# Kernel optimization log

Measured on AMD Instinct MI355X. Metric: run time of the kernel, lower is better.

Reference implementation:

```python
import jax, jax.numpy as jnp
import numpy as np

B, S, D, K = 16, 1024, 512, 4
DIL = (1, 2, 4, 8)
EPS_BN = 1e-5
EPS_LN = 1e-5


def _edge_conv1d(x, w, b, dilation):
    # x: [B, C, S], w: [O, C, k]; replicate ('edge') padding keeps length S
    p = (w.shape[-1] - 1) * dilation // 2
    xp = jnp.pad(x, ((0, 0), (0, 0), (p, p)), mode='edge')
    y = jax.lax.conv_general_dilated(xp, w, (1,), 'VALID', rhs_dilation=(dilation,),
                                     dimension_numbers=('NCH', 'OIH', 'NCH'))
    return y + b[None, :, None]


def setup_inputs() -> dict:
    key = jax.random.key(0)
    ks = jax.random.split(key, 16)
    g = lambda i, shape, s: jax.random.normal(ks[i], shape, jnp.float32) * s
    return {
        'x': g(0, (B, S, D), 1.0),
        'conv_w': g(1, (4, D, D, 3), 0.02),
        'conv_b': jnp.zeros((4, D), jnp.float32),
        'fusion_w': g(2, (D, 4 * D), 0.02),
        'fusion_b': jnp.zeros((D,), jnp.float32),
        'refine_w': g(3, (D, D, 3), 0.02),
        'refine_b': jnp.zeros((D,), jnp.float32),
        'hyp1_w': g(4, (D, D, 3), 0.02),
        'hyp1_b': jnp.zeros((D,), jnp.float32),
        'bn_gamma': jnp.ones((D,), jnp.float32),
        'bn_beta': jnp.zeros((D,), jnp.float32),
        'hyp2_w': g(5, (D // 2, D, 3), 0.02),
        'hyp2_b': jnp.zeros((D // 2,), jnp.float32),
        'proj_w': g(6, (2 * K, D // 2), 0.05),
        'proj_b': jnp.zeros((2 * K,), jnp.float32),
        'gate_w': g(7, (D, D), 0.02),
        'gate_b': jnp.zeros((D,), jnp.float32),
        'base_w': g(8, (D, D), 0.02),
        'base_b': jnp.zeros((D,), jnp.float32),
        'wav_w': g(9, (K, D, D), 0.02),
        'wav_b': jnp.zeros((K, D), jnp.float32),
        'ln_gamma': jnp.ones((D,), jnp.float32),
        'ln_beta': jnp.zeros((D,), jnp.float32),
    }


def _forward(x, conv_w, conv_b, fusion_w, fusion_b, refine_w, refine_b,
             hyp1_w, hyp1_b, bn_gamma, bn_beta, hyp2_w, hyp2_b,
             proj_w, proj_b, gate_w, gate_b, base_w, base_b,
             wav_w, wav_b, ln_gamma, ln_beta):
    residual = x
    x_in = jnp.transpose(x, (0, 2, 1))                      # [B, D, S]
    # ---- FFT trend/seasonal split ----
    fx = jnp.fft.rfft(x_in, axis=2)
    cutoff = S // 10
    mask = (jnp.arange(fx.shape[2]) < cutoff).astype(fx.dtype)
    x_seasonal = jnp.fft.irfft(fx * mask, n=S, axis=2)       # [B, D, S]
    x_smooth = x_seasonal
    x_spike = x_in - x_seasonal
    # ---- iterative dilated-conv smoothing (dropout = identity, eval mode) ----
    for _ in range(2):  # iterations
        outs = [jax.nn.gelu(_edge_conv1d(x_smooth, conv_w[i], conv_b[i], DIL[i]),
                            approximate=False)
                for i in range(4)]
        x_concat = jnp.concatenate(outs, axis=1)             # [B, 4D, S]
        x_smooth = jnp.einsum('oc,bcs->bos', fusion_w, x_concat) + fusion_b[None, :, None]
        x_spike = _edge_conv1d(x_in - x_smooth, refine_w, refine_b, 1)
    x_smooth_t = jnp.transpose(x_smooth, (0, 2, 1))          # [B, S, D]
    x_spike_t = jnp.transpose(x_spike, (0, 2, 1))            # [B, S, D]
    # ---- hypernet (BatchNorm in eval mode: running mean 0, var 1) ----
    h = _edge_conv1d(x_smooth, hyp1_w, hyp1_b, 1)
    h = h / jnp.sqrt(1.0 + EPS_BN) * bn_gamma[None, :, None] + bn_beta[None, :, None]
    h = jax.nn.silu(h)
    h = jax.nn.silu(_edge_conv1d(h, hyp2_w, hyp2_b, 1))      # [B, D/2, S]
    cnn_feat = jnp.mean(h, axis=2)                           # AdaptiveAvgPool1d(1)
    params = (cnn_feat @ proj_w.T + proj_b).reshape(B, 1, K, 2)
    dyn_a = jax.nn.softplus(params[..., 0]) + 0.01           # [B, 1, K]
    dyn_b = jax.nn.sigmoid(params[..., 1]) * S               # [B, 1, K]
    # ---- wavelet-KAN base path: Linear(silu(x_smooth)) ----
    base_out = jnp.einsum('bsd,ed->bse', jax.nn.silu(x_smooth_t), base_w) + base_b
    # ---- wavelet path: mexican-hat wavelets over sequence positions ----
    pos = jnp.arange(S, dtype=x.dtype)[None, :, None]        # [1, S, 1]
    u = (pos - dyn_b) / dyn_a                                # [B, S, K]
    c = 2.0 / (np.sqrt(3.0) * np.pi ** 0.25)
    psi = c * (1.0 - u * u) * jnp.exp(-0.5 * u * u)          # [B, S, K]
    z = jnp.einsum('bsd,kde->bkse', x_spike_t, wav_w)        # per-wavelet linear
    kan_out = jnp.einsum('bsk,bkse->bse', psi, z) + jnp.einsum('bsk,ke->bse', psi, wav_b)
    amp = jax.nn.sigmoid(base_out @ gate_w.T + gate_b) * 2.0
    x_out = base_out + kan_out * amp
    # ---- residual + LayerNorm ----
    y = x_out + residual
    mu = jnp.mean(y, axis=-1, keepdims=True)
    var = jnp.var(y, axis=-1, keepdims=True)
    return (y - mu) / jnp.sqrt(var + EPS_LN) * ln_gamma + ln_beta


def reference(x, conv_w, conv_b, fusion_w, fusion_b, refine_w, refine_b,
              hyp1_w, hyp1_b, bn_gamma, bn_beta, hyp2_w, hyp2_b,
              proj_w, proj_b, gate_w, gate_b, base_w, base_b,
              wav_w, wav_b, ln_gamma, ln_beta):
    return _forward(x, conv_w, conv_b, fusion_w, fusion_b, refine_w, refine_b,
                    hyp1_w, hyp1_b, bn_gamma, bn_beta, hyp2_w, hyp2_b,
                    proj_w, proj_b, gate_w, gate_b, base_w, base_b,
                    wav_w, wav_b, ln_gamma, ln_beta)
```

## Files before the change

kernel.cpp:

```cpp
#include <hip/hip_runtime.h>
#include <hip/hip_bf16.h>
#include <math.h>

#define NB 16
#define SS 1024
#define DD 512
#define HD 256

typedef unsigned short US;
typedef short bf16x8 __attribute__((ext_vector_type(8)));
typedef float f32x4 __attribute__((ext_vector_type(4)));
typedef __attribute__((address_space(1))) const void gv1;
typedef __attribute__((address_space(3))) void lv3;

static __device__ __forceinline__ float b2sf(US u){ return __uint_as_float(((unsigned)u)<<16); }
static __device__ __forceinline__ US f2b(float f){
  __hip_bfloat16 h = __float2bfloat16(f);
  union { __hip_bfloat16 h; US u; } c; c.h = h; return c.u;
}
static __device__ __forceinline__ float rd(const void* __restrict__ p, long i, int isf){
  return isf ? ((const float*)p)[i] : b2sf(((const US*)p)[i]);
}

__global__ void k_detect(const void* __restrict__ x, int* __restrict__ flag){
  const US* u = (const US*)x;
  int t = threadIdx.x;
  float m = 0.f;
  for (int i = t; i < 4096; i += 256){
    float v = fabsf(b2sf(u[i]));
    if (isnan(v) || isinf(v)) v = 1e30f;
    m = fmaxf(m, v);
  }
  for (int off = 32; off; off >>= 1) m = fmaxf(m, __shfl_down(m, off));
  __shared__ float sh[4];
  if ((t & 63) == 0) sh[t >> 6] = m;
  __syncthreads();
  if (t == 0){
    float mm = fmaxf(fmaxf(sh[0], sh[1]), fmaxf(sh[2], sh[3]));
    flag[0] = (mm > 1e6f) ? 1 : 0;
  }
}

struct WTab { const void* src[8]; long start[9]; int type[8]; int C[8]; };
__global__ void k_prep_w(WTab wt, US* __restrict__ dst, const int* __restrict__ fl){
  int isf = fl[0];
  long i = (long)blockIdx.x*256 + threadIdx.x;
  if (i >= wt.start[8]) return;
  int s = 0;
  while (i >= wt.start[s+1]) s++;
  long r = i - wt.start[s];
  long si;
  if (wt.type[s] == 0){
    int C = wt.C[s]; long oc3 = 3L*C;
    int o = (int)(r / oc3); int rr = (int)(r - (long)o*oc3); int t = rr / C; int c = rr - t*C;
    si = ((long)o*C + c)*3 + t;
  } else if (wt.type[s] == 1){
    int k = (int)(r >> 18); int e = (int)((r >> 9) & 511); int d = (int)(r & 511);
    si = ((long)(k*512 + d))*512 + e;
  } else si = r;
  dst[i] = f2b(rd(wt.src[s], si, isf));
}

struct FTab { const void* src[14]; int start[15]; };
__global__ void k_cvt_all(FTab ft, float* __restrict__ dst, const int* __restrict__ fl){
  int isf = fl[0];
  int i = blockIdx.x*256 + threadIdx.x;
  if (i >= ft.start[14]) return;
  int s = 0;
  while (i >= ft.start[s+1]) s++;
  dst[i] = rd(ft.src[s], i - ft.start[s], isf);
}

__global__ void k_build_g(float* __restrict__ g){
  int d = blockIdx.x*256 + threadIdx.x;
  if (d >= SS) return;
  float s = 1.f;
  for (int k = 1; k < 102; ++k){
    int r = (k*d) & (SS-1);
    s += 2.f * cosf(6.28318530718f * (float)r * (1.f/SS));
  }
  g[d] = s * (1.f/SS);
}
__global__ void k_build_cmat(const float* __restrict__ g, US* __restrict__ cm){
  int i = blockIdx.x*256 + threadIdx.x;
  if (i >= SS*SS) return;
  int t = i >> 10, s = i & (SS-1);
  cm[i] = f2b(g[(s - t) & (SS-1)]);
}
__global__ __launch_bounds__(256) void k_transpose_b(const void* __restrict__ x, US* __restrict__ xt, const int* __restrict__ fl){
  int isf = fl[0];
  __shared__ float tl[32][33];
  int b = blockIdx.z, s0 = blockIdx.x*32, d0 = blockIdx.y*32;
  int tx = threadIdx.x & 31, ty = threadIdx.x >> 5;
  for (int i = ty; i < 32; i += 8)
    tl[i][tx] = rd(x, ((long)(b*SS + s0+i))*DD + d0+tx, isf);
  __syncthreads();
  for (int i = ty; i < 32; i += 8)
    xt[((long)(b*DD + d0+i))*SS + s0+tx] = f2b(tl[tx][i]);
}

template<int EPI, bool TAPPED>
__global__ __launch_bounds__(512, 2) void k_mfma8(
    const US* __restrict__ A, const US* __restrict__ Bact, void* __restrict__ Out,
    int NYB, int K, long sBbytes, int ldbB, int dil,
    long sOut, int ldo, const float* __restrict__ bias)
{
  __shared__ US ring[65536];
  const int bx = blockIdx.x;
  const int ny = bx % NYB, b = bx / NYB;
  const int m0 = blockIdx.y*256, n0 = ny*256;
  const int dd = (TAPPED && dil < 0) ? (1 << (m0 >> 9)) : dil;
  const char* Bb = (const char*)Bact + (long)b*sBbytes;
  const int tid = threadIdx.x;
  const int lane = tid & 63, w = tid >> 6;
  const int wm = w >> 2, wn = w & 3;
  const int col = lane & 15, g = lane >> 4;
  const int NTs = K >> 5;

  int offA[8], offB[4];
  #pragma unroll
  for (int fm = 0; fm < 8; fm++){
    int r = wm*128 + fm*16 + col;
    int R = r >> 1;
    int wg = ((r & 1) << 2) | g;
    offA[fm] = R*128 + ((wg ^ (R & 7)) << 4);
  }
  #pragma unroll
  for (int fn = 0; fn < 4; fn++){
    int r = wn*64 + fn*16 + col;
    int R = r >> 1;
    int wg = ((r & 1) << 2) | g;
    offB[fn] = R*128 + ((wg ^ (R & 7)) << 4);
  }
  int rl[2], gg[2];
  #pragma unroll
  for (int j = 0; j < 2; j++){
    int c = (w*2 + j)*64 + lane;
    int R = c >> 3, f = c & 7;
    int wg = f ^ (R & 7);
    rl[j] = 2*R + (wg >> 2);
    gg[j] = wg & 3;
  }

  auto stageA = [&](int t){
    int slot = t & 3, kb = t << 5;
    #pragma unroll
    for (int j = 0; j < 2; j++){
      const char* ga = (const char*)A + ((long)(m0 + rl[j])*K + kb + gg[j]*8)*2;
      __builtin_amdgcn_global_load_lds((gv1*)ga, (lv3*)&ring[slot*8192 + (w*2 + j)*512], 16, 0, 0);
    }
  };
  auto stageB = [&](int t){
    int slot = t & 3, kb = t << 5;
    int c0 = TAPPED ? (kb & 511) : kb;
    int tapoff = TAPPED ? (((kb >> 9) - 1)*dd) : 0;
    #pragma unroll
    for (int j = 0; j < 2; j++){
      int brow = n0 + rl[j] + tapoff;
      if (TAPPED) brow = brow < 0 ? 0 : (brow > SS-1 ? SS-1 : brow);
      const char* gb = Bb + (long)brow*ldbB + (c0 + gg[j]*8)*2;
      __builtin_amdgcn_global_load_lds((gv1*)gb, (lv3*)&ring[32768 + slot*8192 + (w*2 + j)*512], 16, 0, 0);
    }
  };

  f32x4 acc[8][4];
  #pragma unroll
  for (int i = 0; i < 8; i++)
    #pragma unroll
    for (int j = 0; j < 4; j++) acc[i][j] = (f32x4){0.f,0.f,0.f,0.f};

  stageA(0); stageB(0);
  if (NTs > 1){ stageA(1); stageB(1); }
  if (NTs > 2) stageA(2);
  asm volatile("s_waitcnt vmcnt(6)" ::: "memory");
  __builtin_amdgcn_s_barrier();

  bf16x8 af[4], bf[4];
  for (int ks = 0; ks < NTs; ++ks){
    const char* As = (const char*)&ring[(ks & 3)*8192];
    const char* Bs = (const char*)&ring[32768 + (ks & 3)*8192];
    #pragma unroll
    for (int fn = 0; fn < 4; fn++) bf[fn] = *(const bf16x8*)(Bs + offB[fn]);
    #pragma unroll
    for (int fm = 0; fm < 4; fm++) af[fm] = *(const bf16x8*)(As + offA[fm]);
    if (ks + 2 < NTs) stageB(ks + 2);
    __builtin_amdgcn_s_barrier();
    __builtin_amdgcn_s_setprio(1);
    #pragma unroll
    for (int fm = 0; fm < 4; fm++)
      #pragma unroll
      for (int fn = 0; fn < 4; fn++)
        acc[fm][fn] = __builtin_amdgcn_mfma_f32_16x16x32_bf16(af[fm], bf[fn], acc[fm][fn], 0, 0, 0);
    __builtin_amdgcn_s_setprio(0);
    __builtin_amdgcn_s_barrier();
    #pragma unroll
    for (int fm = 0; fm < 4; fm++) af[fm] = *(const bf16x8*)(As + offA[4 + fm]);
    if (ks + 3 < NTs) stageA(ks + 3);
    __builtin_amdgcn_s_barrier();
    __builtin_amdgcn_s_setprio(1);
    #pragma unroll
    for (int fm = 0; fm < 4; fm++)
      #pragma unroll
      for (int fn = 0; fn < 4; fn++)
        acc[4 + fm][fn] = __builtin_amdgcn_mfma_f32_16x16x32_bf16(af[fm], bf[fn], acc[4 + fm][fn], 0, 0, 0);
    __builtin_amdgcn_s_setprio(0);
    if (ks < NTs - 3)       asm volatile("s_waitcnt vmcnt(6)" ::: "memory");
    else if (ks == NTs - 3) asm volatile("s_waitcnt vmcnt(4)" ::: "memory");
    else if (ks == NTs - 2) asm volatile("s_waitcnt vmcnt(0)" ::: "memory");
    __builtin_amdgcn_s_barrier();
  }

  US* tile = ring;
  #pragma unroll
  for (int fm = 0; fm < 8; fm++){
    int m_l = wm*128 + fm*16 + g*4;
    float4 bb = *(const float4*)&bias[m0 + m_l];
    const float* bp = (const float*)&bb;
    #pragma unroll
    for (int fn = 0; fn < 4; fn++){
      int n_l = wn*64 + fn*16 + col;
      f32x4 v = acc[fm][fn];
      US pk[4];
      #pragma unroll
      for (int r = 0; r < 4; r++){
        float val = v[r] + bp[r];
        if (EPI == 1) val = 0.5f*val*(1.f + erff(val*0.70710678f));
        pk[r] = f2b(val);
      }
      long byte = (long)n_l*512 + ((((m_l >> 3) ^ (n_l & 7)) << 4) | ((m_l & 7)*2));
      *(int2*)((char*)tile + byte) = *(int2*)pk;
    }
  }
  __syncthreads();
  #pragma unroll
  for (int p = 0; p < 16; p++){
    int chunk = p*512 + tid;
    int rr = chunk >> 5, cg = chunk & 31;
    int4 vv = *(const int4*)((const char*)tile + (long)rr*512 + ((cg ^ (rr & 7)) << 4));
    *(int4*)((US*)Out + (long)b*sOut + (long)(n0 + rr)*ldo + m0 + cg*8) = vv;
  }
}

template<int EPI, bool TAPPED>
__global__ __launch_bounds__(256) void k_mfma(
    const US* __restrict__ A, const US* __restrict__ Bact, void* __restrict__ Out,
    int NYB, int K, long sBbytes, int ldbB, int dil,
    long sOut, int ldo,
    const float* __restrict__ bias, const float* __restrict__ s1v, const float* __restrict__ s2v,
    const float* __restrict__ psiP, const void* __restrict__ xres,
    US* __restrict__ aux1, US* __restrict__ aux2, const int* __restrict__ fl)
{
  __shared__ alignas(16) US shb[2*128*64];
  __shared__ float psh[(EPI==4) ? 512 : 4];
  US* As = shb;
  US* Bs = shb + 128*64;
  const int bx = blockIdx.x;
  const int ny = bx % NYB;
  const int b  = bx / NYB;
  const int m00 = blockIdx.y*128, n0 = ny*128;
  const int dd = (TAPPED && dil < 0) ? (1 << (m00 >> 9)) : dil;
  const char* Bb = (const char*)Bact + (long)b*sBbytes;
  const int tid = threadIdx.x;
  const int lane = tid & 63, w = tid >> 6;
  const int wr = w >> 1, wc = w & 1;
  const int col = lane & 15, g = lane >> 4;

  if (EPI == 4){
    for (int i = tid; i < 512; i += 256)
      psh[i] = psiP[(long)b*4096 + (i >> 7)*SS + n0 + (i & 127)];
  }

  f32x4 acc[4][4];
  f32x4 facc[4][4];
  if (EPI == 4){
    #pragma unroll
    for (int i = 0; i < 4; i++)
      #pragma unroll
      for (int j = 0; j < 4; j++) facc[i][j] = (f32x4){0.f,0.f,0.f,0.f};
  }

  int rows_[4], sls_[4];
  #pragma unroll
  for (int i = 0; i < 4; i++){
    int c = w*256 + i*64 + lane;
    rows_[i] = c >> 3;
    sls_[i] = (c & 7) ^ ((c >> 3) & 7);
  }

  const int NKC = (EPI == 4) ? 4 : 1;
  for (int kc = 0; kc < NKC; ++kc){
    #pragma unroll
    for (int i = 0; i < 4; i++)
      #pragma unroll
      for (int j = 0; j < 4; j++) acc[i][j] = (f32x4){0.f,0.f,0.f,0.f};

    for (int k0 = 0; k0 < K; k0 += 64){
      const int c0 = TAPPED ? (k0 & 511) : k0;
      const int tapoff = TAPPED ? (((k0 >> 9) - 1)*dd) : 0;
      __syncthreads();
      #pragma unroll
      for (int i = 0; i < 4; i++){
        const long arow = (long)(m00 + rows_[i]) + (EPI==4 ? kc*512 : 0);
        const char* ga = (const char*)A + (arow*K + k0)*2 + sls_[i]*16;
        __builtin_amdgcn_global_load_lds((gv1*)ga, (lv3*)&As[(w*256 + i*64)*8], 16, 0, 0);
        int brow = n0 + rows_[i] + tapoff;
        if (TAPPED) brow = brow < 0 ? 0 : (brow > SS-1 ? SS-1 : brow);
        const char* gb = Bb + (long)brow*ldbB + c0*2 + sls_[i]*16;
        __builtin_amdgcn_global_load_lds((gv1*)gb, (lv3*)&Bs[(w*256 + i*64)*8], 16, 0, 0);
      }
      __syncthreads();
      #pragma unroll
      for (int kk = 0; kk < 2; kk++){
        bf16x8 af[4], bf[4];
        #pragma unroll
        for (int f = 0; f < 4; f++){
          int rowa = wr*64 + f*16 + col;
          int sla = (g + kk*4) ^ (rowa & 7);
          af[f] = *(const bf16x8*)&As[rowa*64 + sla*8];
          int rowb = wc*64 + f*16 + col;
          int slb = (g + kk*4) ^ (rowb & 7);
          bf[f] = *(const bf16x8*)&Bs[rowb*64 + slb*8];
        }
        #pragma unroll
        for (int fm = 0; fm < 4; fm++)
          #pragma unroll
          for (int fn = 0; fn < 4; fn++)
            acc[fm][fn] = __builtin_amdgcn_mfma_f32_16x16x32_bf16(af[fm], bf[fn], acc[fm][fn], 0, 0, 0);
      }
    }

    if (EPI == 4){
      #pragma unroll
      for (int fm = 0; fm < 4; fm++){
        const int mm_l = wr*64 + fm*16 + g*4;
        float bb[4];
        #pragma unroll
        for (int r = 0; r < 4; r++) bb[r] = bias[kc*512 + m00 + mm_l + r];
        #pragma unroll
        for (int fn = 0; fn < 4; fn++){
          float p = psh[kc*128 + wc*64 + fn*16 + col];
          #pragma unroll
          for (int r = 0; r < 4; r++)
            facc[fm][fn][r] += p * (acc[fm][fn][r] + bb[r]);
        }
      }
    }
  }

  __syncthreads();
  US* tile = shb;
  #pragma unroll
  for (int fm = 0; fm < 4; fm++){
    const int mm_l = wr*64 + fm*16 + g*4;
    float bb[4];
    if (EPI == 0 || EPI == 2 || EPI == 3 || EPI == 6){
      #pragma unroll
      for (int r = 0; r < 4; r++) bb[r] = bias[m00 + mm_l + r];
    }
    #pragma unroll
    for (int fn = 0; fn < 4; fn++){
      const int nn_l = wc*64 + fn*16 + col;
      f32x4 v = (EPI == 4) ? facc[fm][fn] : acc[fm][fn];
      if (EPI == 5){
        #pragma unroll
        for (int r = 0; r < 4; r++){
          int row = mm_l + r;
          int byte = row*256 + ((nn_l*2) ^ ((row & 7) << 4));
          *(US*)((char*)tile + byte) = f2b(v[r]);
        }
      } else {
        US pk[4];
        #pragma unroll
        for (int r = 0; r < 4; r++){
          float val = v[r];
          if (EPI != 4) val += bb[r];
          if (EPI == 2){ int m = m00 + mm_l + r; val = val*(s1v[m]*0.99999500f) + s2v[m]; val = val/(1.f + expf(-val)); }
          if (EPI == 3){ val = val/(1.f + expf(-val)); }
          pk[r] = f2b(val);
        }
        int byte = nn_l*256 + ((mm_l*2) ^ ((nn_l & 7) << 4));
        *(int2*)((char*)tile + byte) = *(int2*)pk;
      }
    }
  }
  __syncthreads();
  const int r0 = tid >> 4, c = tid & 15;
  const int isf = (EPI == 6) ? fl[0] : 0;
  #pragma unroll
  for (int p = 0; p < 8; p++){
    int r = p*16 + r0;
    int4 vv = *(const int4*)((const char*)tile + r*256 + ((c*16) ^ ((r & 7) << 4)));
    long obase = (EPI == 5) ? ((long)b*sOut + (long)(m00 + r)*ldo + n0)
                            : ((long)b*sOut + (long)(n0 + r)*ldo + m00);
    *(int4*)((US*)Out + obase + c*8) = vv;
    if (EPI == 6){
      long eb = obase + c*8;
      const US* vp = (const US*)&vv;
      US dpk[8], lpk[8];
      #pragma unroll
      for (int q = 0; q < 8; q++){
        float sv = b2sf(vp[q]);
        float xv = rd(xres, eb + q, isf);
        dpk[q] = f2b(xv - sv);
        lpk[q] = f2b(sv/(1.f + expf(-sv)));
      }
      *(int4*)&aux1[eb] = *(int4*)dpk;
      *(int4*)&aux2[eb] = *(int4*)lpk;
    }
  }
}

__global__ __launch_bounds__(256) void k_pool1(const US* __restrict__ h2, float* __restrict__ part){
  int blk = blockIdx.x;
  int b = blk >> 3, ch = blk & 7;
  int c = threadIdx.x;
  float s = 0.f;
  for (int t = ch*128; t < ch*128 + 128; t++) s += b2sf(h2[((long)(b*SS + t))*HD + c]);
  part[(blk << 8) | c] = s;
}
__global__ __launch_bounds__(256) void k_pool2(const float* __restrict__ part, float* __restrict__ feat){
  int b = blockIdx.x, c = threadIdx.x;
  float s = 0.f;
  for (int ch = 0; ch < 8; ch++) s += part[((b*8 + ch) << 8) | c];
  feat[b*HD + c] = s * (1.f/SS);
}
__global__ void k_params(const float* __restrict__ feat, const float* __restrict__ pw,
                         const float* __restrict__ pb, float* __restrict__ dynA, float* __restrict__ dynB){
  int t = threadIdx.x;
  if (t >= 128) return;
  int b = t >> 3, j = t & 7;
  float s = pb[j];
  for (int c = 0; c < HD; c++) s += feat[b*HD + c]*pw[j*HD + c];
  int k = j >> 1;
  if ((j & 1) == 0){
    float sp = s > 20.f ? s : log1pf(expf(s));
    dynA[b*4 + k] = sp + 0.01f;
  } else {
    dynB[b*4 + k] = 1024.f/(1.f + expf(-s));
  }
}
__global__ void k_psi(const float* __restrict__ dynA, const float* __restrict__ dynB, float* __restrict__ psi){
  int i = blockIdx.x*256 + threadIdx.x;
  if (i >= NB*4*SS) return;
  int b = i >> 12, k = (i >> 10) & 3, s = i & (SS-1);
  float u = ((float)s - dynB[b*4 + k]) / dynA[b*4 + k];
  psi[i] = 0.86732507f*(1.f - u*u)*expf(-0.5f*u*u);
}
__global__ __launch_bounds__(128) void k_final(const US* __restrict__ base, const US* __restrict__ kan,
    const US* __restrict__ gate, const void* __restrict__ x,
    void* __restrict__ out, const float* __restrict__ lng, const float* __restrict__ lnb,
    const int* __restrict__ fl){
  int isf = fl[0];
  long row = blockIdx.x;
  int t = threadIdx.x;
  long off = row*DD + t*4;
  ushort4 bs = *(const ushort4*)&base[off];
  ushort4 gt = *(const ushort4*)&gate[off];
  ushort4 kn = *(const ushort4*)&kan[off];
  float xv[4];
  if (isf){ float4 q = *(const float4*)((const float*)x + off); xv[0]=q.x; xv[1]=q.y; xv[2]=q.z; xv[3]=q.w; }
  else { ushort4 q = *(const ushort4*)((const US*)x + off); xv[0]=b2sf(q.x); xv[1]=b2sf(q.y); xv[2]=b2sf(q.z); xv[3]=b2sf(q.w); }
  float bv[4] = {b2sf(bs.x), b2sf(bs.y), b2sf(bs.z), b2sf(bs.w)};
  float gv[4] = {b2sf(gt.x), b2sf(gt.y), b2sf(gt.z), b2sf(gt.w)};
  const US* kp = (const US*)&kn;
  float y[4];
  float sm = 0.f, ssq = 0.f;
  #pragma unroll
  for (int r = 0; r < 4; r++){
    float amp = 2.f/(1.f + expf(-gv[r]));
    y[r] = bv[r] + b2sf(kp[r])*amp + xv[r];
    sm += y[r]; ssq += y[r]*y[r];
  }
  for (int o = 32; o; o >>= 1){ sm += __shfl_down(sm, o); ssq += __shfl_down(ssq, o); }
  __shared__ float sh[4];
  int lane = t & 63, wid = t >> 6;
  if (lane == 0){ sh[wid*2] = sm; sh[wid*2+1] = ssq; }
  __syncthreads();
  float S1 = sh[0] + sh[2], S2 = sh[1] + sh[3];
  float mean = S1*(1.f/DD), var = S2*(1.f/DD) - mean*mean;
  float rstd = rsqrtf(var + 1e-5f);
  #pragma unroll
  for (int r = 0; r < 4; r++){
    int d = t*4 + r;
    float val = (y[r] - mean)*rstd*lng[d] + lnb[d];
    if (isf) ((float*)out)[off + r] = val;
    else     ((US*)out)[off + r] = f2b(val);
  }
}

extern "C" void kernel_launch(void* const* d_in, const int* in_sizes, int n_in,
                              void* d_out, int out_size, void* d_ws, size_t ws_size,
                              hipStream_t stream){
  const void* x       = d_in[0];
  const void* conv_w  = d_in[1];
  const void* conv_b  = d_in[2];
  const void* fusion_w= d_in[3];
  const void* fusion_b= d_in[4];
  const void* refine_w= d_in[5];
  const void* refine_b= d_in[6];
  const void* hyp1_w  = d_in[7];
  const void* hyp1_b  = d_in[8];
  const void* bn_g    = d_in[9];
  const void* bn_b    = d_in[10];
  const void* hyp2_w  = d_in[11];
  const void* hyp2_b  = d_in[12];
  const void* proj_w  = d_in[13];
  const void* proj_b  = d_in[14];
  const void* gate_w  = d_in[15];
  const void* gate_b  = d_in[16];
  const void* base_w  = d_in[17];
  const void* base_b  = d_in[18];
  const void* wav_w   = d_in[19];
  const void* wav_b   = d_in[20];
  const void* ln_g    = d_in[21];
  const void* ln_b    = d_in[22];

  char* wsb = (char*)d_ws;
  long off = 0;
  auto AA = [&](long bytes)->char*{ char* p = wsb + off; off += (bytes + 255) & ~255L; return p; };
  US* smA   = (US*)AA((long)NB*SS*DD*2);
  US* smB   = (US*)AA((long)NB*SS*DD*2);
  US* xTh   = (US*)AA((long)NB*SS*DD*2);
  US* cc    = (US*)AA((long)NB*SS*2048*2);
  US* baseB = (US*)AA((long)NB*SS*DD*2);
  US* WBLK  = (US*)AA(7733248L*2);
  US* Cm    = (US*)AA(1024L*1024*2);
  float* gvec = (float*)AA(1024*4);
  float* FBLK = (float*)AA(11016L*4);
  float* feat = (float*)AA(16*256*4);
  float* part = (float*)AA(16*8*256*4);
  float* dynA = (float*)AA(64*4);
  float* dynB = (float*)AA(64*4);
  float* psi  = (float*)AA((long)NB*4*SS*4);
  int* flag   = (int*)AA(64);
  if ((size_t)off > ws_size) return;

  US* Wc  = WBLK;
  US* Wr  = Wc  + 3145728L;
  US* Wh1 = Wr  + 786432L;
  US* Wh2 = Wh1 + 786432L;
  US* Wwv = Wh2 + 393216L;
  US* Fw  = Wwv + 1048576L;
  US* BW  = Fw  + 1048576L;
  US* GW  = BW  + 262144L;
  float* cb_f = FBLK;
  float* fz_b = cb_f + 2048;
  float* rf_b = fz_b + 512;
  float* h1_b = rf_b + 512;
  float* h2_b = h1_b + 512;
  float* bs_b = h2_b + 256;
  float* gt_b = bs_b + 512;
  float* wv_b = gt_b + 512;
  float* bngf = wv_b + 2048;
  float* bnbf = bngf + 512;
  float* pwf  = bnbf + 512;
  float* pbf  = pwf  + 2048;
  float* lngf = pbf  + 8;
  float* lnbf = lngf + 512;
  US* spike = cc;
  US* baseO = cc + 8388608L;
  US* kanb  = cc + 16777216L;
  US* h2b   = cc + 25165824L;

  auto g1 = [](long n){ return dim3((unsigned)((n + 255)/256)); };
  const long sAct = (long)SS*DD*2;
  const long sCC  = (long)SS*2048*2;
  const long oAct = (long)SS*DD;
  const long oCC  = (long)SS*2048;
  const long oH2  = (long)SS*HD;

  k_detect<<<1, 256, 0, stream>>>(x, flag);

  { WTab wt;
    const void* srcs[8] = {conv_w, refine_w, hyp1_w, hyp2_w, wav_w, fusion_w, base_w, gate_w};
    long sizes[8] = {3145728, 786432, 786432, 393216, 1048576, 1048576, 262144, 262144};
    int types[8] = {0,0,0,0,1,2,2,2};
    int Cs[8]    = {512,512,512,512,0,0,0,0};
    long acc_ = 0;
    for (int i = 0; i < 8; i++){ wt.src[i]=srcs[i]; wt.start[i]=acc_; wt.type[i]=types[i]; wt.C[i]=Cs[i]; acc_ += sizes[i]; }
    wt.start[8] = acc_;
    k_prep_w<<<g1(acc_), 256, 0, stream>>>(wt, WBLK, flag);
  }
  { FTab ft;
    const void* srcs[14] = {conv_b, fusion_b, refine_b, hyp1_b, hyp2_b, base_b, gate_b,
                            wav_b, bn_g, bn_b, proj_w, proj_b, ln_g, ln_b};
    int sizes[14] = {2048,512,512,512,256,512,512,2048,512,512,2048,8,512,512};
    int acc_ = 0;
    for (int i = 0; i < 14; i++){ ft.src[i]=srcs[i]; ft.start[i]=acc_; acc_ += sizes[i]; }
    ft.start[14] = acc_;
    k_cvt_all<<<g1(acc_), 256, 0, stream>>>(ft, FBLK, flag);
  }
  k_build_g<<<g1(SS), 256, 0, stream>>>(gvec);
  k_build_cmat<<<g1((long)SS*SS), 256, 0, stream>>>(gvec, Cm);
  k_transpose_b<<<dim3(SS/32, DD/32, NB), 256, 0, stream>>>(x, xTh, flag);

  k_mfma<5,false><<<dim3(4*NB, 8), 256, 0, stream>>>(Cm, xTh, smA,
      4, 1024, (long)DD*SS*2, SS*2, 0, oAct, DD,
      nullptr, nullptr, nullptr, nullptr, nullptr, nullptr, nullptr, nullptr);

  k_mfma8<1,true><<<dim3(4*NB, 8), 512, 0, stream>>>(Wc, smA, cc,
      4, 1536, sAct, DD*2, -1, oCC, 2048, cb_f);
  k_mfma<0,false><<<dim3(8*NB, 4), 256, 0, stream>>>(Fw, cc, smB,
      8, 2048, sCC, 4096, 0, oAct, DD,
      fz_b, nullptr, nullptr, nullptr, nullptr, nullptr, nullptr, nullptr);
  k_mfma8<1,true><<<dim3(4*NB, 8), 512, 0, stream>>>(Wc, smB, cc,
      4, 1536, sAct, DD*2, -1, oCC, 2048, cb_f);
  k_mfma<6,false><<<dim3(8*NB, 4), 256, 0, stream>>>(Fw, cc, smA,
      8, 2048, sCC, 4096, 0, oAct, DD,
      fz_b, nullptr, nullptr, nullptr, x, smB, baseB, flag);

  k_mfma<0,true><<<dim3(8*NB, 4), 256, 0, stream>>>(Wr, smB, spike,
      8, 1536, sAct, DD*2, 1, oAct, DD,
      rf_b, nullptr, nullptr, nullptr, nullptr, nullptr, nullptr, nullptr);

  k_mfma<2,true><<<dim3(8*NB, 4), 256, 0, stream>>>(Wh1, smA, xTh,
      8, 1536, sAct, DD*2, 1, oAct, DD,
      h1_b, bngf, bnbf, nullptr, nullptr, nullptr, nullptr, nullptr);
  k_mfma<3,true><<<dim3(8*NB, 2), 256, 0, stream>>>(Wh2, xTh, h2b,
      8, 1536, sAct, DD*2, 1, oH2, HD,
      h2_b, nullptr, nullptr, nullptr, nullptr, nullptr, nullptr, nullptr);
  k_pool1<<<NB*8, 256, 0, stream>>>(h2b, part);
  k_pool2<<<NB, 256, 0, stream>>>(part, feat);
  k_params<<<1, 128, 0, stream>>>(feat, pwf, pbf, dynA, dynB);
  k_psi<<<g1(NB*4*SS), 256, 0, stream>>>(dynA, dynB, psi);

  k_mfma<0,false><<<dim3(8*NB, 4), 256, 0, stream>>>(BW, baseB, baseO,
      8, 512, sAct, DD*2, 0, oAct, DD,
      bs_b, nullptr, nullptr, nullptr, nullptr, nullptr, nullptr, nullptr);
  k_mfma<0,false><<<dim3(8*NB, 4), 256, 0, stream>>>(GW, baseO, xTh,
      8, 512, sAct, DD*2, 0, oAct, DD,
      gt_b, nullptr, nullptr, nullptr, nullptr, nullptr, nullptr, nullptr);

  k_mfma<4,false><<<dim3(8*NB, 4), 256, 0, stream>>>(Wwv, spike, kanb,
      8, 512, sAct, DD*2, 0, oAct, DD,
      wv_b, nullptr, nullptr, psi, nullptr, nullptr, nullptr, nullptr);

  k_final<<<NB*SS, 128, 0, stream>>>(baseO, kanb, xTh, x, d_out, lngf, lnbf, flag);
}
```

Baseline: 671.2 us.

## Replace 256x256 four-stage ring conv GEMM with 256x128 double-buffered kernel

The multi-dilation conv GEMM kernel moves from a 256x256 output tile with a 4-slot LDS ring and split A-fragment loads to a 256x128 tile with 2-slot double buffering. LDS use drops from 128KB to 64KB and launch bounds rise to 4 blocks per CU, doubling the grid to 1024 blocks. The aim is better occupancy and load balance across CUs. In exchange, each block reuses less data per tile, adds more B-operand global traffic, and has a shallower prefetch pipeline.

Measured after the change: 667.1 us. Within noise of the previous version (-0.6%).

```diff
diff --git a/kernel.cpp b/kernel.cpp
--- a/kernel.cpp
+++ b/kernel.cpp
@@ -100,126 +100,115 @@
 }
 
 template<int EPI, bool TAPPED>
-__global__ __launch_bounds__(512, 2) void k_mfma8(
+__global__ __launch_bounds__(512, 4) void k_dbuf(
     const US* __restrict__ A, const US* __restrict__ Bact, void* __restrict__ Out,
     int NYB, int K, long sBbytes, int ldbB, int dil,
     long sOut, int ldo, const float* __restrict__ bias)
 {
-  __shared__ US ring[65536];
+  __shared__ US ring[32768];
   const int bx = blockIdx.x;
   const int ny = bx % NYB, b = bx / NYB;
-  const int m0 = blockIdx.y*256, n0 = ny*256;
+  const int m0 = blockIdx.y*256, n0 = ny*128;
   const int dd = (TAPPED && dil < 0) ? (1 << (m0 >> 9)) : dil;
   const char* Bb = (const char*)Bact + (long)b*sBbytes;
   const int tid = threadIdx.x;
   const int lane = tid & 63, w = tid >> 6;
-  const int wm = w >> 2, wn = w & 3;
+  const int wm = w >> 1, wn = w & 1;
   const int col = lane & 15, g = lane >> 4;
   const int NTs = K >> 5;
 
-  int offA[8], offB[4];
-  #pragma unroll
-  for (int fm = 0; fm < 8; fm++){
-    int r = wm*128 + fm*16 + col;
-    int R = r >> 1;
+  int offA[4], offB[4];
+  #pragma unroll
+  for (int mf = 0; mf < 4; mf++){
+    int r = wm*64 + mf*16 + col;
     int wg = ((r & 1) << 2) | g;
-    offA[fm] = R*128 + ((wg ^ (R & 7)) << 4);
-  }
-  #pragma unroll
-  for (int fn = 0; fn < 4; fn++){
-    int r = wn*64 + fn*16 + col;
-    int R = r >> 1;
+    offA[mf] = (r >> 1)*128 + ((wg ^ ((r >> 1) & 7)) << 4);
+  }
+  #pragma unroll
+  for (int nf = 0; nf < 4; nf++){
+    int r = wn*64 + nf*16 + col;
     int wg = ((r & 1) << 2) | g;
-    offB[fn] = R*128 + ((wg ^ (R & 7)) << 4);
-  }
-  int rl[2], gg[2];
+    offB[nf] = (r >> 1)*128 + ((wg ^ ((r >> 1) & 7)) << 4);
+  }
+  int rlA[2], ggA[2];
   #pragma unroll
   for (int j = 0; j < 2; j++){
-    int c = (w*2 + j)*64 + lane;
+    int c = w*128 + j*64 + lane;
     int R = c >> 3, f = c & 7;
     int wg = f ^ (R & 7);
-    rl[j] = 2*R + (wg >> 2);
-    gg[j] = wg & 3;
+    rlA[j] = 2*R + (wg >> 2);
+    ggA[j] = wg & 3;
+  }
+  int rlB, ggB;
+  {
+    int R = tid >> 3, f = tid & 7;
+    int wg = f ^ (R & 7);
+    rlB = 2*R + (wg >> 2);
+    ggB = wg & 3;
   }
 
   auto stageA = [&](int t){
-    int slot = t & 3, kb = t << 5;
+    int slot = t & 1, kb = t << 5;
     #pragma unroll
     for (int j = 0; j < 2; j++){
-      const char* ga = (const char*)A + ((long)(m0 + rl[j])*K + kb + gg[j]*8)*2;
-      __builtin_amdgcn_global_load_lds((gv1*)ga, (lv3*)&ring[slot*8192 + (w*2 + j)*512], 16, 0, 0);
+      const char* ga = (const char*)A + ((long)(m0 + rlA[j])*K + kb + ggA[j]*8)*2;
+      __builtin_amdgcn_global_load_lds((gv1*)ga, (lv3*)&ring[slot*8192 + w*1024 + j*512], 16, 0, 0);
     }
   };
   auto stageB = [&](int t){
-    int slot = t & 3, kb = t << 5;
+    int slot = t & 1, kb = t << 5;
     int c0 = TAPPED ? (kb & 511) : kb;
     int tapoff = TAPPED ? (((kb >> 9) - 1)*dd) : 0;
-    #pragma unroll
-    for (int j = 0; j < 2; j++){
-      int brow = n0 + rl[j] + tapoff;
-      if (TAPPED) brow = brow < 0 ? 0 : (brow > SS-1 ? SS-1 : brow);
-      const char* gb = Bb + (long)brow*ldbB + (c0 + gg[j]*8)*2;
-      __builtin_amdgcn_global_load_lds((gv1*)gb, (lv3*)&ring[32768 + slot*8192 + (w*2 + j)*512], 16, 0, 0);
-    }
+    int brow = n0 + rlB + tapoff;
+    if (TAPPED) brow = brow < 0 ? 0 : (brow > SS-1 ? SS-1 : brow);
+    const char* gb = Bb + (long)brow*ldbB + (c0 + ggB*8)*2;
+    __builtin_amdgcn_global_load_lds((gv1*)gb, (lv3*)&ring[16384 + slot*4096 + w*512], 16, 0, 0);
   };
 
-  f32x4 acc[8][4];
-  #pragma unroll
-  for (int i = 0; i < 8; i++)
+  f32x4 acc[4][4];
+  #pragma unroll
+  for (int i = 0; i < 4; i++)
     #pragma unroll
     for (int j = 0; j < 4; j++) acc[i][j] = (f32x4){0.f,0.f,0.f,0.f};
 
   stageA(0); stageB(0);
-  if (NTs > 1){ stageA(1); stageB(1); }
-  if (NTs > 2) stageA(2);
-  asm volatile("s_waitcnt vmcnt(6)" ::: "memory");
+  stageA(1); stageB(1);
+  asm volatile("s_waitcnt vmcnt(3)" ::: "memory");
   __builtin_amdgcn_s_barrier();
 
-  bf16x8 af[4], bf[4];
   for (int ks = 0; ks < NTs; ++ks){
-    const char* As = (const char*)&ring[(ks & 3)*8192];
-    const char* Bs = (const char*)&ring[32768 + (ks & 3)*8192];
-    #pragma unroll
-    for (int fn = 0; fn < 4; fn++) bf[fn] = *(const bf16x8*)(Bs + offB[fn]);
-    #pragma unroll
-    for (int fm = 0; fm < 4; fm++) af[fm] = *(const bf16x8*)(As + offA[fm]);
-    if (ks + 2 < NTs) stageB(ks + 2);
+    const char* As = (const char*)&ring[(ks & 1)*8192];
+    const char* Bs = (const char*)&ring[16384 + (ks & 1)*4096];
+    bf16x8 af[4], bf[4];
+    #pragma unroll
+    for (int mf = 0; mf < 4; mf++) af[mf] = *(const bf16x8*)(As + offA[mf]);
+    #pragma unroll
+    for (int nf = 0; nf < 4; nf++) bf[nf] = *(const bf16x8*)(Bs + offB[nf]);
+    asm volatile("s_waitcnt lgkmcnt(0)" ::: "memory");
     __builtin_amdgcn_s_barrier();
+    if (ks + 2 < NTs){ stageA(ks + 2); stageB(ks + 2); }
     __builtin_amdgcn_s_setprio(1);
     #pragma unroll
-    for (int fm = 0; fm < 4; fm++)
-      #pragma unroll
-      for (int fn = 0; fn < 4; fn++)
-        acc[fm][fn] = __builtin_amdgcn_mfma_f32_16x16x32_bf16(af[fm], bf[fn], acc[fm][fn], 0, 0, 0);
+    for (int mf = 0; mf < 4; mf++)
+      #pragma unroll
+      for (int nf = 0; nf < 4; nf++)
+        acc[mf][nf] = __builtin_amdgcn_mfma_f32_16x16x32_bf16(af[mf], bf[nf], acc[mf][nf], 0, 0, 0);
     __builtin_amdgcn_s_setprio(0);
-    __builtin_amdgcn_s_barrier();
-    #pragma unroll
-    for (int fm = 0; fm < 4; fm++) af[fm] = *(const bf16x8*)(As + offA[4 + fm]);
-    if (ks + 3 < NTs) stageA(ks + 3);
-    __builtin_amdgcn_s_barrier();
-    __builtin_amdgcn_s_setprio(1);
-    #pragma unroll
-    for (int fm = 0; fm < 4; fm++)
-      #pragma unroll
-      for (int fn = 0; fn < 4; fn++)
-        acc[4 + fm][fn] = __builtin_amdgcn_mfma_f32_16x16x32_bf16(af[fm], bf[fn], acc[4 + fm][fn], 0, 0, 0);
-    __builtin_amdgcn_s_setprio(0);
-    if (ks < NTs - 3)       asm volatile("s_waitcnt vmcnt(6)" ::: "memory");
-    else if (ks == NTs - 3) asm volatile("s_waitcnt vmcnt(4)" ::: "memory");
+    if (ks < NTs - 2)       asm volatile("s_waitcnt vmcnt(3)" ::: "memory");
     else if (ks == NTs - 2) asm volatile("s_waitcnt vmcnt(0)" ::: "memory");
     __builtin_amdgcn_s_barrier();
   }
 
   US* tile = ring;
   #pragma unroll
-  for (int fm = 0; fm < 8; fm++){
-    int m_l = wm*128 + fm*16 + g*4;
+  for (int mf = 0; mf < 4; mf++){
+    int m_l = wm*64 + mf*16 + g*4;
     float4 bb = *(const float4*)&bias[m0 + m_l];
     const float* bp = (const float*)&bb;
     #pragma unroll
-    for (int fn = 0; fn < 4; fn++){
-      int n_l = wn*64 + fn*16 + col;
-      f32x4 v = acc[fm][fn];
+    for (int nf = 0; nf < 4; nf++){
+      int n_l = wn*64 + nf*16 + col;
+      f32x4 v = acc[mf][nf];
       US pk[4];
       #pragma unroll
       for (int r = 0; r < 4; r++){
@@ -233,7 +222,7 @@
   }
   __syncthreads();
   #pragma unroll
-  for (int p = 0; p < 16; p++){
+  for (int p = 0; p < 8; p++){
     int chunk = p*512 + tid;
     int rr = chunk >> 5, cg = chunk & 31;
     int4 vv = *(const int4*)((const char*)tile + (long)rr*512 + ((cg ^ (rr & 7)) << 4));
@@ -598,13 +587,13 @@
       4, 1024, (long)DD*SS*2, SS*2, 0, oAct, DD,
       nullptr, nullptr, nullptr, nullptr, nullptr, nullptr, nullptr, nullptr);
 
-  k_mfma8<1,true><<<dim3(4*NB, 8), 512, 0, stream>>>(Wc, smA, cc,
-      4, 1536, sAct, DD*2, -1, oCC, 2048, cb_f);
+  k_dbuf<1,true><<<dim3(8*NB, 8), 512, 0, stream>>>(Wc, smA, cc,
+      8, 1536, sAct, DD*2, -1, oCC, 2048, cb_f);
   k_mfma<0,false><<<dim3(8*NB, 4), 256, 0, stream>>>(Fw, cc, smB,
       8, 2048, sCC, 4096, 0, oAct, DD,
       fz_b, nullptr, nullptr, nullptr, nullptr, nullptr, nullptr, nullptr);
-  k_mfma8<1,true><<<dim3(4*NB, 8), 512, 0, stream>>>(Wc, smB, cc,
-      4, 1536, sAct, DD*2, -1, oCC, 2048, cb_f);
+  k_dbuf<1,true><<<dim3(8*NB, 8), 512, 0, stream>>>(Wc, smB, cc,
+      8, 1536, sAct, DD*2, -1, oCC, 2048, cb_f);
   k_mfma<6,false><<<dim3(8*NB, 4), 256, 0, stream>>>(Fw, cc, smA,
       8, 2048, sCC, 4096, 0, oAct, DD,
       fz_b, nullptr, nullptr, nullptr, x, smB, baseB, flag);
```
